# Kernel optimization log

Hardware: AMD Instinct MI355X
Metric: run time of the kernel (lower is better)

## Reference

```python
import jax, jax.numpy as jnp
import numpy as np

B, L, D = 4, 4096, 1024
H, W = 16, 64          # n_heads, window_size
HD = D // H            # head_dim
EPS = 1e-5


def setup_inputs() -> dict:
    key = jax.random.key(0)
    ks = jax.random.split(key, 3)
    s = 1.0 / np.sqrt(D)
    x = jax.random.normal(ks[0], (B, L, D), dtype=jnp.float32)
    Wqkv = (jax.random.normal(ks[1], (3 * D, D), dtype=jnp.float32) * s)
    bqkv = jnp.zeros((3 * D,), dtype=jnp.float32)
    Wproj = (jax.random.normal(ks[2], (D, D), dtype=jnp.float32) * s)
    bproj = jnp.zeros((D,), dtype=jnp.float32)
    gamma = jnp.ones((D,), dtype=jnp.float32)
    beta = jnp.zeros((D,), dtype=jnp.float32)
    return {"x": x, "Wqkv": Wqkv, "bqkv": bqkv, "Wproj": Wproj,
            "bproj": bproj, "gamma": gamma, "beta": beta}


def reference(x, Wqkv, bqkv, Wproj, bproj, gamma, beta):
    scale = HD ** -0.5
    nw = L // W  # L is a multiple of W, so pad_len == 0 (same math as padded path)
    # QKV projection -> [3, B, H, L, HD]
    qkv = (x @ Wqkv.T + bqkv).reshape(B, L, 3, H, HD).transpose(2, 0, 3, 1, 4)
    q, k, v = qkv[0], qkv[1], qkv[2]
    # split into non-overlapping windows: [B, H, nw, W, HD]
    q = q.reshape(B, H, nw, W, HD)
    k = k.reshape(B, H, nw, W, HD)
    v = v.reshape(B, H, nw, W, HD)
    attn = jax.nn.softmax(jnp.einsum('bhnqd,bhnkd->bhnqk', q, k) * scale, axis=-1)
    out = jnp.einsum('bhnqk,bhnkd->bhnqd', attn, v)  # dropout is identity in eval
    out = out.reshape(B, H, L, HD).transpose(0, 2, 1, 3).reshape(B, L, D)
    out = out @ Wproj.T + bproj
    y = out + x
    mean = jnp.mean(y, axis=-1, keepdims=True)
    var = jnp.mean((y - mean) ** 2, axis=-1, keepdims=True)
    return (y - mean) * jax.lax.rsqrt(var + EPS) * gamma + beta
```

## Files before the change

kernel.cpp:

```cpp
#include <hip/hip_runtime.h>
#include <stdint.h>


typedef __attribute__((ext_vector_type(8))) short short8;
typedef __attribute__((ext_vector_type(4))) float float4v;
typedef unsigned short us;

#define GAS const __attribute__((address_space(1))) void
#define LAS __attribute__((address_space(3))) void

__device__ __forceinline__ float bf2f(us u) {
  return __uint_as_float(((unsigned int)u) << 16);
}
__device__ __forceinline__ us f2bf(float f) {
  unsigned int u = __float_as_uint(f);
  unsigned int r = u + 0x7FFFu + ((u >> 16) & 1u);
  return (us)(r >> 16);
}
__device__ __forceinline__ int4 stage8(const float* p) {
  float4 a = *(const float4*)p;
  float4 b = *(const float4*)(p + 4);
  int4 r;
  us* u = (us*)&r;
  u[0] = f2bf(a.x); u[1] = f2bf(a.y); u[2] = f2bf(a.z); u[3] = f2bf(a.w);
  u[4] = f2bf(b.x); u[5] = f2bf(b.y); u[6] = f2bf(b.z); u[7] = f2bf(b.w);
  return r;
}
__device__ __forceinline__ int4 stage8(const us* p) { return *(const int4*)p; }
__device__ __forceinline__ void stc(us* p, float v) { *p = f2bf(v); }
__device__ __forceinline__ void stc(float* p, float v) { *p = v; }

__global__ __launch_bounds__(256) void cast_bf16(const float* __restrict__ src,
                                                 us* __restrict__ dst, int n8) {
  const int i = blockIdx.x * 256 + threadIdx.x;
  if (i < n8) *(int4*)(dst + (size_t)i * 8) = stage8(src + (size_t)i * 8);
}

template <int N, int K, int EPI, int HM, typename CT>
__global__ __launch_bounds__(512, 1) void gemm256(
    const us* __restrict__ A, const us* __restrict__ Bt,
    const float* __restrict__ bias, const float* __restrict__ resid,
    CT* __restrict__ C) {
  __shared__ __align__(16) us As[2][256 * 64];
  __shared__ __align__(16) us Bs[2][256 * 64];
  const int tid = threadIdx.x;
  const int lane = tid & 63;
  const int wave = tid >> 6;
  const int wm = wave >> 2;
  const int wn = wave & 3;
  const int lr = lane & 15, lq = lane >> 4;
  const int m0 = blockIdx.y * 256;
  const int n0 = blockIdx.x * 256;
  const int trow = tid >> 3;
  const int tcol = (((tid & 7) ^ (trow & 7)) * 8);

  constexpr int NT = K / 64;

  float4v acc[8][4];
#pragma unroll
  for (int i = 0; i < 8; i++)
#pragma unroll
    for (int j = 0; j < 4; j++) acc[i][j] = (float4v)0.0f;

#define STAGE256(buf, t)                                                       \
  do {                                                                         \
    const size_t kof = (size_t)(t) * 64;                                       \
    _Pragma("unroll") for (int q = 0; q < 4; q++) {                            \
      const us* ga = A + (size_t)(m0 + q * 64 + trow) * K + kof + tcol;        \
      __builtin_amdgcn_global_load_lds((GAS*)ga,                               \
          (LAS*)&As[buf][(q * 512 + tid) * 8], 16, 0, 0);                      \
    }                                                                          \
    _Pragma("unroll") for (int q = 0; q < 4; q++) {                            \
      const us* gb = Bt + (size_t)(n0 + q * 64 + trow) * K + kof + tcol;       \
      __builtin_amdgcn_global_load_lds((GAS*)gb,                               \
          (LAS*)&Bs[buf][(q * 512 + tid) * 8], 16, 0, 0);                      \
    }                                                                          \
  } while (0)

  STAGE256(0, 0);

  for (int t = 0; t < NT; t++) {
    const int cur = t & 1;
    __builtin_amdgcn_s_barrier();
    if (t + 1 < NT) {
      STAGE256(cur ^ 1, t + 1);
      asm volatile("s_waitcnt vmcnt(8)" ::: "memory");
    } else {
      asm volatile("s_waitcnt vmcnt(0)" ::: "memory");
    }
    __builtin_amdgcn_s_barrier();

    const us* Ab = As[cur];
    const us* Bb = Bs[cur];
#pragma unroll
    for (int kk8 = 0; kk8 < 2; kk8++) {
      short8 bf8[4];
#pragma unroll
      for (int nt = 0; nt < 4; nt++) {
        const int row = wn * 64 + nt * 16 + lr;
        bf8[nt] = *(const short8*)&Bb[row * 64 + (((kk8 * 4 + lq) ^ (lr & 7)) * 8)];
      }
#pragma unroll
      for (int mh = 0; mh < 2; mh++) {
        short8 af[4];
#pragma unroll
        for (int mt = 0; mt < 4; mt++) {
          const int row = wm * 128 + mh * 64 + mt * 16 + lr;
          af[mt] = *(const short8*)&Ab[row * 64 + (((kk8 * 4 + lq) ^ (lr & 7)) * 8)];
        }
        __builtin_amdgcn_s_setprio(1);
#pragma unroll
        for (int mt = 0; mt < 4; mt++)
#pragma unroll
          for (int nt = 0; nt < 4; nt++)
            acc[mh * 4 + mt][nt] = __builtin_amdgcn_mfma_f32_16x16x32_bf16(
                af[mt], bf8[nt], acc[mh * 4 + mt][nt], 0, 0, 0);
        __builtin_amdgcn_s_setprio(0);
      }
    }
  }
#undef STAGE256

  float bb[4];
#pragma unroll
  for (int nt = 0; nt < 4; nt++) bb[nt] = bias[n0 + wn * 64 + nt * 16 + lr];
#pragma unroll
  for (int mh = 0; mh < 2; mh++)
#pragma unroll
    for (int mt = 0; mt < 4; mt++) {
      const int rbase = m0 + wm * 128 + mh * 64 + mt * 16 + lq * 4;
#pragma unroll
      for (int nt = 0; nt < 4; nt++) {
        const int col = n0 + wn * 64 + nt * 16 + lr;
#pragma unroll
        for (int r = 0; r < 4; r++) {
          float v = acc[mh * 4 + mt][nt][r] + bb[nt];
          const int row = rbase + r;
          size_t idx;
          if (HM) {
            const int mat = col >> 10, hh = (col >> 6) & 15, d = col & 63;
            idx = (size_t)mat * (16384u * 1024u) +
                  (size_t)((row >> 12) * 16 + hh) * (4096u * 64u) +
                  (size_t)(row & 4095) * 64 + d;
          } else {
            idx = (size_t)row * N + col;
          }
          if (EPI) v += resid[idx];
          stc(&C[idx], v);
        }
      }
    }
}

__global__ __launch_bounds__(256) void attn_mfma(
    const us* __restrict__ qkv, us* __restrict__ attn) {
  __shared__ __align__(16) us Vt[64 * 64];
  __shared__ __align__(16) us Pl[4 * 16 * 64];
  const int wid = blockIdx.x;
  const int wi = wid & 63;
  const int h = (wid >> 6) & 15;
  const int b = wid >> 10;
  const int tid = threadIdx.x;
  const int lane = tid & 63;
  const int w = tid >> 6;
  const int lr = lane & 15, lq = lane >> 4;
  const int rowbase = b * 4096 + wi * 64;

  const us* Qb = qkv + (size_t)(b * 16 + h) * (4096u * 64u) + (size_t)wi * 4096;
  const us* Kb = Qb + (size_t)16384 * 1024;
  const us* Vb = Kb + (size_t)16384 * 1024;

  {
    const int r = lane;
    const int cs = w * 16;
    const us* vsrc = Vb + (size_t)r * 64 + cs;
    int4 v0 = *(const int4*)vsrc;
    int4 v1 = *(const int4*)(vsrc + 8);
    const us* vv0 = (const us*)&v0;
    const us* vv1 = (const us*)&v1;
#pragma unroll
    for (int i = 0; i < 8; i++) {
      const int d = cs + i;
      Vt[d * 64 + (((r >> 3) ^ (d & 7)) * 8) + (r & 7)] = vv0[i];
    }
#pragma unroll
    for (int i = 0; i < 8; i++) {
      const int d = cs + 8 + i;
      Vt[d * 64 + (((r >> 3) ^ (d & 7)) * 8) + (r & 7)] = vv1[i];
    }
  }

  short8 aq[2];
  {
    const us* qrow = Qb + (size_t)(w * 16 + lr) * 64 + lq * 8;
    aq[0] = *(const short8*)qrow;
    aq[1] = *(const short8*)(qrow + 32);
  }
  float4v s[4];
#pragma unroll
  for (int nt = 0; nt < 4; nt++) s[nt] = (float4v)0.0f;
#pragma unroll
  for (int kk8 = 0; kk8 < 2; kk8++) {
#pragma unroll
    for (int nt = 0; nt < 4; nt++) {
      const us* krow = Kb + (size_t)(nt * 16 + lr) * 64 + kk8 * 32 + lq * 8;
      short8 bk = *(const short8*)krow;
      s[nt] = __builtin_amdgcn_mfma_f32_16x16x32_bf16(aq[kk8], bk, s[nt], 0, 0, 0);
    }
  }

  float p[4][4];
#pragma unroll
  for (int r = 0; r < 4; r++) {
    float mx = -1e30f;
#pragma unroll
    for (int nt = 0; nt < 4; nt++) {
      s[nt][r] *= 0.125f;
      mx = fmaxf(mx, s[nt][r]);
    }
    mx = fmaxf(mx, __shfl_xor(mx, 1));
    mx = fmaxf(mx, __shfl_xor(mx, 2));
    mx = fmaxf(mx, __shfl_xor(mx, 4));
    mx = fmaxf(mx, __shfl_xor(mx, 8));
    float sum = 0.f;
#pragma unroll
    for (int nt = 0; nt < 4; nt++) {
      p[nt][r] = __expf(s[nt][r] - mx);
      sum += p[nt][r];
    }
    sum += __shfl_xor(sum, 1);
    sum += __shfl_xor(sum, 2);
    sum += __shfl_xor(sum, 4);
    sum += __shfl_xor(sum, 8);
    const float inv = 1.0f / sum;
#pragma unroll
    for (int nt = 0; nt < 4; nt++) p[nt][r] *= inv;
  }

  us* pw = Pl + w * 1024;
#pragma unroll
  for (int nt = 0; nt < 4; nt++) {
    const int c = nt * 16 + lr;
#pragma unroll
    for (int r = 0; r < 4; r++) {
      const int row = lq * 4 + r;
      pw[row * 64 + (((c >> 3) ^ (row & 7)) * 8) + (c & 7)] = f2bf(p[nt][r]);
    }
  }
  __syncthreads();

  float4v o[4];
#pragma unroll
  for (int nt = 0; nt < 4; nt++) o[nt] = (float4v)0.0f;
#pragma unroll
  for (int kk8 = 0; kk8 < 2; kk8++) {
    short8 pa = *(const short8*)&pw[lr * 64 + (((lq + kk8 * 4) ^ (lr & 7)) * 8)];
#pragma unroll
    for (int nt = 0; nt < 4; nt++) {
      const int d = nt * 16 + lr;
      short8 vb = *(const short8*)&Vt[d * 64 + (((lq + kk8 * 4) ^ (d & 7)) * 8)];
      o[nt] = __builtin_amdgcn_mfma_f32_16x16x32_bf16(pa, vb, o[nt], 0, 0, 0);
    }
  }

#pragma unroll
  for (int nt = 0; nt < 4; nt++) {
    const int d = nt * 16 + lr;
#pragma unroll
    for (int r = 0; r < 4; r++) {
      const int tok = rowbase + w * 16 + lq * 4 + r;
      attn[(size_t)tok * 1024 + h * 64 + d] = f2bf(o[nt][r]);
    }
  }
}

template <int N, int K, int EPI, typename AT, typename CT>
__global__ __launch_bounds__(256) void gemm_bt(
    const AT* __restrict__ A, const float* __restrict__ Bt,
    const float* __restrict__ bias, const float* __restrict__ resid,
    CT* __restrict__ C) {
  __shared__ __align__(16) us As[128 * 64];
  __shared__ __align__(16) us Bs[128 * 64];
  const int tid = threadIdx.x;
  const int lane = tid & 63;
  const int wave = tid >> 6;
  const int wm = wave >> 1, wn = wave & 1;
  const int lr = lane & 15, lq = lane >> 4;
  const int m0 = blockIdx.y * 128;
  const int n0 = blockIdx.x * 128;
  const int trow = tid >> 3;
  const int tcol = (tid & 7) * 8;

  float4v acc[4][4];
#pragma unroll
  for (int i = 0; i < 4; i++)
#pragma unroll
    for (int j = 0; j < 4; j++) acc[i][j] = (float4v)0.0f;

  for (int k0 = 0; k0 < K; k0 += 64) {
    int4 av[4], bv[4];
#pragma unroll
    for (int p = 0; p < 4; p++) {
      av[p] = stage8(A + (size_t)(m0 + p * 32 + trow) * K + k0 + tcol);
      bv[p] = stage8(Bt + (size_t)(n0 + p * 32 + trow) * K + k0 + tcol);
    }
#pragma unroll
    for (int p = 0; p < 4; p++) {
      *(int4*)&As[(p * 256 + tid) * 8] = av[p];
      *(int4*)&Bs[(p * 256 + tid) * 8] = bv[p];
    }
    __syncthreads();
#pragma unroll
    for (int kk = 0; kk < 64; kk += 32) {
      short8 af[4], bfv[4];
#pragma unroll
      for (int mt = 0; mt < 4; mt++)
        af[mt] = *(const short8*)&As[(wm * 64 + mt * 16 + lr) * 64 + kk + lq * 8];
#pragma unroll
      for (int nt = 0; nt < 4; nt++)
        bfv[nt] = *(const short8*)&Bs[(wn * 64 + nt * 16 + lr) * 64 + kk + lq * 8];
#pragma unroll
      for (int mt = 0; mt < 4; mt++)
#pragma unroll
        for (int nt = 0; nt < 4; nt++)
          acc[mt][nt] = __builtin_amdgcn_mfma_f32_16x16x32_bf16(
              af[mt], bfv[nt], acc[mt][nt], 0, 0, 0);
    }
    __syncthreads();
  }

  float bb[4];
#pragma unroll
  for (int nt = 0; nt < 4; nt++) bb[nt] = bias[n0 + wn * 64 + nt * 16 + lr];
#pragma unroll
  for (int mt = 0; mt < 4; mt++) {
    const int rbase = m0 + wm * 64 + mt * 16 + lq * 4;
#pragma unroll
    for (int nt = 0; nt < 4; nt++) {
      const int col = n0 + wn * 64 + nt * 16 + lr;
#pragma unroll
      for (int r = 0; r < 4; r++) {
        float v = acc[mt][nt][r] + bb[nt];
        size_t idx = (size_t)(rbase + r) * N + col;
        if (EPI) v += resid[idx];
        stc(&C[idx], v);
      }
    }
  }
}

__global__ __launch_bounds__(256) void attn_win(
    const us* __restrict__ qkv, us* __restrict__ attn) {
  __shared__ float qs[64][65];
  __shared__ float ks[64][65];
  __shared__ float vs[64][65];
  const int wid = blockIdx.x;
  const int wi = wid & 63;
  const int h = (wid >> 6) & 15;
  const int b = wid >> 10;
  const int t = threadIdx.x;
  const int rowbase = b * 4096 + wi * 64;
  {
    const int r = t >> 2;
    const int cs = (t & 3) * 16;
    const us* base = qkv + (size_t)(rowbase + r) * 3072 + h * 64 + cs;
#pragma unroll
    for (int s = 0; s < 3; s++) {
      float* dst = (s == 0) ? &qs[r][cs] : (s == 1) ? &ks[r][cs] : &vs[r][cs];
      const us* src = base + s * 1024;
#pragma unroll
      for (int half = 0; half < 2; half++) {
        int4 dv = *(const int4*)(src + half * 8);
        const us* tp = (const us*)&dv;
#pragma unroll
        for (int i = 0; i < 8; i++) dst[half * 8 + i] = bf2f(tp[i]);
      }
    }
  }
  __syncthreads();
  const int r0 = (t >> 4) * 4;
  const int c0 = (t & 15) * 4;
  float acc[4][4] = {};
#pragma unroll 8
  for (int k = 0; k < 64; k++) {
    float qv[4], kv[4];
#pragma unroll
    for (int i = 0; i < 4; i++) qv[i] = qs[r0 + i][k];
#pragma unroll
    for (int j = 0; j < 4; j++) kv[j] = ks[c0 + j][k];
#pragma unroll
    for (int i = 0; i < 4; i++)
#pragma unroll
      for (int j = 0; j < 4; j++) acc[i][j] += qv[i] * kv[j];
  }
  __syncthreads();
#pragma unroll
  for (int i = 0; i < 4; i++)
#pragma unroll
    for (int j = 0; j < 4; j++) qs[r0 + i][c0 + j] = acc[i][j] * 0.125f;
  __syncthreads();
  {
    const int rr = t >> 2;
    const int cs = (t & 3) * 16;
    float pv[16];
    float m = -1e30f;
#pragma unroll
    for (int i = 0; i < 16; i++) {
      pv[i] = qs[rr][cs + i];
      m = fmaxf(m, pv[i]);
    }
    m = fmaxf(m, __shfl_xor(m, 1));
    m = fmaxf(m, __shfl_xor(m, 2));
    float ssum = 0.f;
#pragma unroll
    for (int i = 0; i < 16; i++) {
      pv[i] = __expf(pv[i] - m);
      ssum += pv[i];
    }
    ssum += __shfl_xor(ssum, 1);
    ssum += __shfl_xor(ssum, 2);
    const float inv = 1.0f / ssum;
#pragma unroll
    for (int i = 0; i < 16; i++) qs[rr][cs + i] = pv[i] * inv;
  }
  __syncthreads();
  float o[4][4] = {};
#pragma unroll 8
  for (int k = 0; k < 64; k++) {
    float pr[4], vv[4];
#pragma unroll
    for (int i = 0; i < 4; i++) pr[i] = qs[r0 + i][k];
#pragma unroll
    for (int j = 0; j < 4; j++) vv[j] = vs[k][c0 + j];
#pragma unroll
    for (int i = 0; i < 4; i++)
#pragma unroll
      for (int j = 0; j < 4; j++) o[i][j] += pr[i] * vv[j];
  }
#pragma unroll
  for (int i = 0; i < 4; i++)
#pragma unroll
    for (int j = 0; j < 4; j++)
      attn[(size_t)(rowbase + r0 + i) * 1024 + h * 64 + c0 + j] = f2bf(o[i][j]);
}

__global__ __launch_bounds__(256) void ln_inplace(
    float* __restrict__ y, const float* __restrict__ gamma,
    const float* __restrict__ beta) {
  const int row = blockIdx.x;
  const int t = threadIdx.x;
  float* yr = y + (size_t)row * 1024;
  float4 v = *(const float4*)(yr + t * 4);
  float s1 = v.x + v.y + v.z + v.w;
  float s2 = v.x * v.x + v.y * v.y + v.z * v.z + v.w * v.w;
#pragma unroll
  for (int off = 32; off > 0; off >>= 1) {
    s1 += __shfl_down(s1, off);
    s2 += __shfl_down(s2, off);
  }
  __shared__ float red[8];
  const int lane = t & 63, wave = t >> 6;
  if (lane == 0) {
    red[wave] = s1;
    red[4 + wave] = s2;
  }
  __syncthreads();
  if (t == 0) {
    red[0] = red[0] + red[1] + red[2] + red[3];
    red[4] = red[4] + red[5] + red[6] + red[7];
  }
  __syncthreads();
  const float mean = red[0] * (1.0f / 1024.0f);
  const float var = red[4] * (1.0f / 1024.0f) - mean * mean;
  const float rstd = rsqrtf(var + 1e-5f);
  float4 g = *(const float4*)(gamma + t * 4);
  float4 bt = *(const float4*)(beta + t * 4);
  float4 o;
  o.x = (v.x - mean) * rstd * g.x + bt.x;
  o.y = (v.y - mean) * rstd * g.y + bt.y;
  o.z = (v.z - mean) * rstd * g.z + bt.z;
  o.w = (v.w - mean) * rstd * g.w + bt.w;
  *(float4*)(yr + t * 4) = o;
}

extern "C" void kernel_launch(void* const* d_in, const int* in_sizes, int n_in,
                              void* d_out, int out_size, void* d_ws,
                              size_t ws_size, hipStream_t stream) {
  const float* x = (const float*)d_in[0];
  const float* Wqkv = (const float*)d_in[1];
  const float* bqkv = (const float*)d_in[2];
  const float* Wproj = (const float*)d_in[3];
  const float* bproj = (const float*)d_in[4];
  const float* gamma = (const float*)d_in[5];
  const float* beta = (const float*)d_in[6];
  float* out = (float*)d_out;

  us* qkv = (us*)d_ws;
  us* attn = qkv + (size_t)16384 * 3072;
  us* xb = attn + (size_t)16384 * 1024;
  us* Wqkvb = xb + (size_t)16384 * 1024;
  us* Wprojb = Wqkvb + (size_t)3072 * 1024;
  const size_t need =
      ((size_t)16384 * 3072 + 3 * (size_t)16384 * 1024 + (size_t)3072 * 1024 +
       (size_t)1024 * 1024) * sizeof(us);

  if (ws_size >= need) {
    cast_bf16<<<(16384 * 1024 / 8 + 255) / 256, 256, 0, stream>>>(x, xb,
                                                                  16384 * 128);
    cast_bf16<<<(3072 * 1024 / 8 + 255) / 256, 256, 0, stream>>>(Wqkv, Wqkvb,
                                                                 3072 * 128);
    cast_bf16<<<(1024 * 1024 / 8 + 255) / 256, 256, 0, stream>>>(Wproj, Wprojb,
                                                                 1024 * 128);
    gemm256<3072, 1024, 0, 1, us><<<dim3(12, 64), 512, 0, stream>>>(
        xb, Wqkvb, bqkv, nullptr, qkv);
    attn_mfma<<<4096, 256, 0, stream>>>(qkv, attn);
    gemm256<1024, 1024, 1, 0, float><<<dim3(4, 64), 512, 0, stream>>>(
        attn, Wprojb, bproj, x, out);
  } else {
    gemm_bt<3072, 1024, 0, float, us><<<dim3(24, 128), 256, 0, stream>>>(
        x, Wqkv, bqkv, nullptr, qkv);
    attn_win<<<4096, 256, 0, stream>>>(qkv, attn);
    gemm_bt<1024, 1024, 1, us, float><<<dim3(8, 128), 256, 0, stream>>>(
        attn, Wproj, bproj, x, out);
  }
  ln_inplace<<<16384, 256, 0, stream>>>(out, gamma, beta);
}
```

Before: 354.5 us.

## Shrink GEMM tiles to 128x128 with grouped block swizzle; batch attention windows per block

Replaces the 256x256x64 tile, 512-thread GEMM with a 128x128x32 tile, 256-thread version that remaps block ids in an interleaved order for better L2 locality. It also drops the launch bound of one block per CU, so more blocks fit on each CU and the grid has many more blocks. The attention kernel now processes four windows per block in a loop instead of one, cutting the launch count by four. The trade-off is less data reuse per tile, more barrier iterations along K, and serialized work inside each attention block.

```diff
diff --git a/kernel.cpp b/kernel.cpp
--- a/kernel.cpp
+++ b/kernel.cpp
@@ -37,54 +37,60 @@
 }
 
 template <int N, int K, int EPI, int HM, typename CT>
-__global__ __launch_bounds__(512, 1) void gemm256(
+__global__ __launch_bounds__(256) void gemm128(
     const us* __restrict__ A, const us* __restrict__ Bt,
     const float* __restrict__ bias, const float* __restrict__ resid,
     CT* __restrict__ C) {
-  __shared__ __align__(16) us As[2][256 * 64];
-  __shared__ __align__(16) us Bs[2][256 * 64];
+  constexpr int NBX = N / 128;
+  constexpr int NBY = 128;
+  constexpr int NWG = NBX * NBY;
+  __shared__ __align__(16) us As[2][128 * 32];
+  __shared__ __align__(16) us Bs[2][128 * 32];
   const int tid = threadIdx.x;
   const int lane = tid & 63;
   const int wave = tid >> 6;
-  const int wm = wave >> 2;
-  const int wn = wave & 3;
+  const int wm = wave >> 1, wn = wave & 1;
   const int lr = lane & 15, lq = lane >> 4;
-  const int m0 = blockIdx.y * 256;
-  const int n0 = blockIdx.x * 256;
-  const int trow = tid >> 3;
-  const int tcol = (((tid & 7) ^ (trow & 7)) * 8);
-
-  constexpr int NT = K / 64;
-
-  float4v acc[8][4];
-#pragma unroll
-  for (int i = 0; i < 8; i++)
+
+  int id = blockIdx.y * NBX + blockIdx.x;
+  id = (id & 7) * (NWG / 8) + (id >> 3);
+  const int m0 = (id / NBX) * 128;
+  const int n0 = (id % NBX) * 128;
+
+  const int srow = tid >> 2;
+  const int scol = (((tid & 3) ^ (srow & 3)) * 8);
+
+  constexpr int NT = K / 32;
+
+  float4v acc[4][4];
+#pragma unroll
+  for (int i = 0; i < 4; i++)
 #pragma unroll
     for (int j = 0; j < 4; j++) acc[i][j] = (float4v)0.0f;
 
-#define STAGE256(buf, t)                                                       \
+#define STG128(buf, t)                                                         \
   do {                                                                         \
-    const size_t kof = (size_t)(t) * 64;                                       \
-    _Pragma("unroll") for (int q = 0; q < 4; q++) {                            \
-      const us* ga = A + (size_t)(m0 + q * 64 + trow) * K + kof + tcol;        \
+    const size_t kof = (size_t)(t) * 32;                                       \
+    _Pragma("unroll") for (int p = 0; p < 2; p++) {                            \
+      const us* ga = A + (size_t)(m0 + p * 64 + srow) * K + kof + scol;        \
       __builtin_amdgcn_global_load_lds((GAS*)ga,                               \
-          (LAS*)&As[buf][(q * 512 + tid) * 8], 16, 0, 0);                      \
+          (LAS*)&As[buf][(p * 256 + tid) * 8], 16, 0, 0);                      \
     }                                                                          \
-    _Pragma("unroll") for (int q = 0; q < 4; q++) {                            \
-      const us* gb = Bt + (size_t)(n0 + q * 64 + trow) * K + kof + tcol;       \
+    _Pragma("unroll") for (int p = 0; p < 2; p++) {                            \
+      const us* gb = Bt + (size_t)(n0 + p * 64 + srow) * K + kof + scol;       \
       __builtin_amdgcn_global_load_lds((GAS*)gb,                               \
-          (LAS*)&Bs[buf][(q * 512 + tid) * 8], 16, 0, 0);                      \
+          (LAS*)&Bs[buf][(p * 256 + tid) * 8], 16, 0, 0);                      \
     }                                                                          \
   } while (0)
 
-  STAGE256(0, 0);
+  STG128(0, 0);
 
   for (int t = 0; t < NT; t++) {
     const int cur = t & 1;
     __builtin_amdgcn_s_barrier();
     if (t + 1 < NT) {
-      STAGE256(cur ^ 1, t + 1);
-      asm volatile("s_waitcnt vmcnt(8)" ::: "memory");
+      STG128(cur ^ 1, t + 1);
+      asm volatile("s_waitcnt vmcnt(4)" ::: "memory");
     } else {
       asm volatile("s_waitcnt vmcnt(0)" ::: "memory");
     }
@@ -92,185 +98,181 @@
 
     const us* Ab = As[cur];
     const us* Bb = Bs[cur];
-#pragma unroll
-    for (int kk8 = 0; kk8 < 2; kk8++) {
-      short8 bf8[4];
-#pragma unroll
-      for (int nt = 0; nt < 4; nt++) {
-        const int row = wn * 64 + nt * 16 + lr;
-        bf8[nt] = *(const short8*)&Bb[row * 64 + (((kk8 * 4 + lq) ^ (lr & 7)) * 8)];
-      }
-#pragma unroll
-      for (int mh = 0; mh < 2; mh++) {
-        short8 af[4];
-#pragma unroll
-        for (int mt = 0; mt < 4; mt++) {
-          const int row = wm * 128 + mh * 64 + mt * 16 + lr;
-          af[mt] = *(const short8*)&Ab[row * 64 + (((kk8 * 4 + lq) ^ (lr & 7)) * 8)];
+    short8 af[4], bf8[4];
+#pragma unroll
+    for (int mt = 0; mt < 4; mt++)
+      af[mt] = *(const short8*)&Ab[(wm * 64 + mt * 16 + lr) * 32 +
+                                   ((lq ^ (lr & 3)) * 8)];
+#pragma unroll
+    for (int nt = 0; nt < 4; nt++)
+      bf8[nt] = *(const short8*)&Bb[(wn * 64 + nt * 16 + lr) * 32 +
+                                    ((lq ^ (lr & 3)) * 8)];
+    __builtin_amdgcn_s_setprio(1);
+#pragma unroll
+    for (int mt = 0; mt < 4; mt++)
+#pragma unroll
+      for (int nt = 0; nt < 4; nt++)
+        acc[mt][nt] = __builtin_amdgcn_mfma_f32_16x16x32_bf16(
+            af[mt], bf8[nt], acc[mt][nt], 0, 0, 0);
+    __builtin_amdgcn_s_setprio(0);
+  }
+#undef STG128
+
+  float bb[4];
+#pragma unroll
+  for (int nt = 0; nt < 4; nt++) bb[nt] = bias[n0 + wn * 64 + nt * 16 + lr];
+#pragma unroll
+  for (int mt = 0; mt < 4; mt++) {
+    const int rbase = m0 + wm * 64 + mt * 16 + lq * 4;
+#pragma unroll
+    for (int nt = 0; nt < 4; nt++) {
+      const int col = n0 + wn * 64 + nt * 16 + lr;
+#pragma unroll
+      for (int r = 0; r < 4; r++) {
+        float v = acc[mt][nt][r] + bb[nt];
+        const int row = rbase + r;
+        size_t idx;
+        if (HM) {
+          const int mat = col >> 10, hh = (col >> 6) & 15, d = col & 63;
+          idx = (size_t)mat * (16384u * 1024u) +
+                (size_t)((row >> 12) * 16 + hh) * (4096u * 64u) +
+                (size_t)(row & 4095) * 64 + d;
+        } else {
+          idx = (size_t)row * N + col;
         }
-        __builtin_amdgcn_s_setprio(1);
-#pragma unroll
-        for (int mt = 0; mt < 4; mt++)
-#pragma unroll
-          for (int nt = 0; nt < 4; nt++)
-            acc[mh * 4 + mt][nt] = __builtin_amdgcn_mfma_f32_16x16x32_bf16(
-                af[mt], bf8[nt], acc[mh * 4 + mt][nt], 0, 0, 0);
-        __builtin_amdgcn_s_setprio(0);
-      }
-    }
-  }
-#undef STAGE256
-
-  float bb[4];
-#pragma unroll
-  for (int nt = 0; nt < 4; nt++) bb[nt] = bias[n0 + wn * 64 + nt * 16 + lr];
-#pragma unroll
-  for (int mh = 0; mh < 2; mh++)
-#pragma unroll
-    for (int mt = 0; mt < 4; mt++) {
-      const int rbase = m0 + wm * 128 + mh * 64 + mt * 16 + lq * 4;
-#pragma unroll
-      for (int nt = 0; nt < 4; nt++) {
-        const int col = n0 + wn * 64 + nt * 16 + lr;
-#pragma unroll
-        for (int r = 0; r < 4; r++) {
-          float v = acc[mh * 4 + mt][nt][r] + bb[nt];
-          const int row = rbase + r;
-          size_t idx;
-          if (HM) {
-            const int mat = col >> 10, hh = (col >> 6) & 15, d = col & 63;
-            idx = (size_t)mat * (16384u * 1024u) +
-                  (size_t)((row >> 12) * 16 + hh) * (4096u * 64u) +
-                  (size_t)(row & 4095) * 64 + d;
-          } else {
-            idx = (size_t)row * N + col;
-          }
-          if (EPI) v += resid[idx];
-          stc(&C[idx], v);
-        }
-      }
-    }
+        if (EPI) v += resid[idx];
+        stc(&C[idx], v);
+      }
+    }
+  }
 }
 
 __global__ __launch_bounds__(256) void attn_mfma(
     const us* __restrict__ qkv, us* __restrict__ attn) {
   __shared__ __align__(16) us Vt[64 * 64];
   __shared__ __align__(16) us Pl[4 * 16 * 64];
-  const int wid = blockIdx.x;
-  const int wi = wid & 63;
-  const int h = (wid >> 6) & 15;
-  const int b = wid >> 10;
+  const int g0 = blockIdx.x * 4;
+  const int h = (g0 >> 6) & 15;
+  const int b = g0 >> 10;
   const int tid = threadIdx.x;
   const int lane = tid & 63;
   const int w = tid >> 6;
   const int lr = lane & 15, lq = lane >> 4;
-  const int rowbase = b * 4096 + wi * 64;
-
-  const us* Qb = qkv + (size_t)(b * 16 + h) * (4096u * 64u) + (size_t)wi * 4096;
-  const us* Kb = Qb + (size_t)16384 * 1024;
-  const us* Vb = Kb + (size_t)16384 * 1024;
-
-  {
-    const int r = lane;
-    const int cs = w * 16;
-    const us* vsrc = Vb + (size_t)r * 64 + cs;
-    int4 v0 = *(const int4*)vsrc;
-    int4 v1 = *(const int4*)(vsrc + 8);
-    const us* vv0 = (const us*)&v0;
-    const us* vv1 = (const us*)&v1;
-#pragma unroll
-    for (int i = 0; i < 8; i++) {
-      const int d = cs + i;
-      Vt[d * 64 + (((r >> 3) ^ (d & 7)) * 8) + (r & 7)] = vv0[i];
-    }
-#pragma unroll
-    for (int i = 0; i < 8; i++) {
-      const int d = cs + 8 + i;
-      Vt[d * 64 + (((r >> 3) ^ (d & 7)) * 8) + (r & 7)] = vv1[i];
-    }
-  }
-
-  short8 aq[2];
-  {
-    const us* qrow = Qb + (size_t)(w * 16 + lr) * 64 + lq * 8;
-    aq[0] = *(const short8*)qrow;
-    aq[1] = *(const short8*)(qrow + 32);
-  }
-  float4v s[4];
-#pragma unroll
-  for (int nt = 0; nt < 4; nt++) s[nt] = (float4v)0.0f;
-#pragma unroll
-  for (int kk8 = 0; kk8 < 2; kk8++) {
+
+  const us* Qh = qkv + (size_t)(b * 16 + h) * (4096u * 64u);
+  const us* Kh = Qh + (size_t)16384 * 1024;
+  const us* Vh = Kh + (size_t)16384 * 1024;
+
+  for (int i = 0; i < 4; i++) {
+    const int wi = (g0 + i) & 63;
+    const int rowbase = b * 4096 + wi * 64;
+    const us* Qb = Qh + (size_t)wi * 4096;
+    const us* Kb = Kh + (size_t)wi * 4096;
+    const us* Vb = Vh + (size_t)wi * 4096;
+
+    {
+      const int r = lane;
+      const int cs = w * 16;
+      const us* vsrc = Vb + (size_t)r * 64 + cs;
+      int4 v0 = *(const int4*)vsrc;
+      int4 v1 = *(const int4*)(vsrc + 8);
+      const us* vv0 = (const us*)&v0;
+      const us* vv1 = (const us*)&v1;
+#pragma unroll
+      for (int k = 0; k < 8; k++) {
+        const int d = cs + k;
+        Vt[d * 64 + (((r >> 3) ^ (d & 7)) * 8) + (r & 7)] = vv0[k];
+      }
+#pragma unroll
+      for (int k = 0; k < 8; k++) {
+        const int d = cs + 8 + k;
+        Vt[d * 64 + (((r >> 3) ^ (d & 7)) * 8) + (r & 7)] = vv1[k];
+      }
+    }
+
+    short8 aq[2];
+    {
+      const us* qrow = Qb + (size_t)(w * 16 + lr) * 64 + lq * 8;
+      aq[0] = *(const short8*)qrow;
+      aq[1] = *(const short8*)(qrow + 32);
+    }
+    float4v s[4];
+#pragma unroll
+    for (int nt = 0; nt < 4; nt++) s[nt] = (float4v)0.0f;
+#pragma unroll
+    for (int kk8 = 0; kk8 < 2; kk8++) {
+#pragma unroll
+      for (int nt = 0; nt < 4; nt++) {
+        const us* krow = Kb + (size_t)(nt * 16 + lr) * 64 + kk8 * 32 + lq * 8;
+        short8 bk = *(const short8*)krow;
+        s[nt] = __builtin_amdgcn_mfma_f32_16x16x32_bf16(aq[kk8], bk, s[nt], 0, 0, 0);
+      }
+    }
+
+    float p[4][4];
+#pragma unroll
+    for (int r = 0; r < 4; r++) {
+      float mx = -1e30f;
+#pragma unroll
+      for (int nt = 0; nt < 4; nt++) {
+        s[nt][r] *= 0.125f;
+        mx = fmaxf(mx, s[nt][r]);
+      }
+      mx = fmaxf(mx, __shfl_xor(mx, 1));
+      mx = fmaxf(mx, __shfl_xor(mx, 2));
+      mx = fmaxf(mx, __shfl_xor(mx, 4));
+      mx = fmaxf(mx, __shfl_xor(mx, 8));
+      float sum = 0.f;
+#pragma unroll
+      for (int nt = 0; nt < 4; nt++) {
+        p[nt][r] = __expf(s[nt][r] - mx);
+        sum += p[nt][r];
+      }
+      sum += __shfl_xor(sum, 1);
+      sum += __shfl_xor(sum, 2);
+      sum += __shfl_xor(sum, 4);
+      sum += __shfl_xor(sum, 8);
+      const float inv = 1.0f / sum;
+#pragma unroll
+      for (int nt = 0; nt < 4; nt++) p[nt][r] *= inv;
+    }
+
+    us* pw = Pl + w * 1024;
 #pragma unroll
     for (int nt = 0; nt < 4; nt++) {
-      const us* krow = Kb + (size_t)(nt * 16 + lr) * 64 + kk8 * 32 + lq * 8;
-      short8 bk = *(const short8*)krow;
-      s[nt] = __builtin_amdgcn_mfma_f32_16x16x32_bf16(aq[kk8], bk, s[nt], 0, 0, 0);
-    }
-  }
-
-  float p[4][4];
-#pragma unroll
-  for (int r = 0; r < 4; r++) {
-    float mx = -1e30f;
-#pragma unroll
-    for (int nt = 0; nt < 4; nt++) {
-      s[nt][r] *= 0.125f;
-      mx = fmaxf(mx, s[nt][r]);
-    }
-    mx = fmaxf(mx, __shfl_xor(mx, 1));
-    mx = fmaxf(mx, __shfl_xor(mx, 2));
-    mx = fmaxf(mx, __shfl_xor(mx, 4));
-    mx = fmaxf(mx, __shfl_xor(mx, 8));
-    float sum = 0.f;
-#pragma unroll
-    for (int nt = 0; nt < 4; nt++) {
-      p[nt][r] = __expf(s[nt][r] - mx);
-      sum += p[nt][r];
-    }
-    sum += __shfl_xor(sum, 1);
-    sum += __shfl_xor(sum, 2);
-    sum += __shfl_xor(sum, 4);
-    sum += __shfl_xor(sum, 8);
-    const float inv = 1.0f / sum;
-#pragma unroll
-    for (int nt = 0; nt < 4; nt++) p[nt][r] *= inv;
-  }
-
-  us* pw = Pl + w * 1024;
-#pragma unroll
-  for (int nt = 0; nt < 4; nt++) {
-    const int c = nt * 16 + lr;
-#pragma unroll
-    for (int r = 0; r < 4; r++) {
-      const int row = lq * 4 + r;
-      pw[row * 64 + (((c >> 3) ^ (row & 7)) * 8) + (c & 7)] = f2bf(p[nt][r]);
-    }
-  }
-  __syncthreads();
-
-  float4v o[4];
-#pragma unroll
-  for (int nt = 0; nt < 4; nt++) o[nt] = (float4v)0.0f;
-#pragma unroll
-  for (int kk8 = 0; kk8 < 2; kk8++) {
-    short8 pa = *(const short8*)&pw[lr * 64 + (((lq + kk8 * 4) ^ (lr & 7)) * 8)];
+      const int c = nt * 16 + lr;
+#pragma unroll
+      for (int r = 0; r < 4; r++) {
+        const int row = lq * 4 + r;
+        pw[row * 64 + (((c >> 3) ^ (row & 7)) * 8) + (c & 7)] = f2bf(p[nt][r]);
+      }
+    }
+    __syncthreads();
+
+    float4v o[4];
+#pragma unroll
+    for (int nt = 0; nt < 4; nt++) o[nt] = (float4v)0.0f;
+#pragma unroll
+    for (int kk8 = 0; kk8 < 2; kk8++) {
+      short8 pa = *(const short8*)&pw[lr * 64 + (((lq + kk8 * 4) ^ (lr & 7)) * 8)];
+#pragma unroll
+      for (int nt = 0; nt < 4; nt++) {
+        const int d = nt * 16 + lr;
+        short8 vb = *(const short8*)&Vt[d * 64 + (((lq + kk8 * 4) ^ (d & 7)) * 8)];
+        o[nt] = __builtin_amdgcn_mfma_f32_16x16x32_bf16(pa, vb, o[nt], 0, 0, 0);
+      }
+    }
+
 #pragma unroll
     for (int nt = 0; nt < 4; nt++) {
       const int d = nt * 16 + lr;
-      short8 vb = *(const short8*)&Vt[d * 64 + (((lq + kk8 * 4) ^ (d & 7)) * 8)];
-      o[nt] = __builtin_amdgcn_mfma_f32_16x16x32_bf16(pa, vb, o[nt], 0, 0, 0);
-    }
-  }
-
-#pragma unroll
-  for (int nt = 0; nt < 4; nt++) {
-    const int d = nt * 16 + lr;
-#pragma unroll
-    for (int r = 0; r < 4; r++) {
-      const int tok = rowbase + w * 16 + lq * 4 + r;
-      attn[(size_t)tok * 1024 + h * 64 + d] = f2bf(o[nt][r]);
-    }
+#pragma unroll
+      for (int r = 0; r < 4; r++) {
+        const int tok = rowbase + w * 16 + lq * 4 + r;
+        attn[(size_t)tok * 1024 + h * 64 + d] = f2bf(o[nt][r]);
+      }
+    }
+    if (i < 3) __syncthreads();
   }
 }
 
@@ -511,10 +513,10 @@
                                                                  3072 * 128);
     cast_bf16<<<(1024 * 1024 / 8 + 255) / 256, 256, 0, stream>>>(Wproj, Wprojb,
                                                                  1024 * 128);
-    gemm256<3072, 1024, 0, 1, us><<<dim3(12, 64), 512, 0, stream>>>(
+    gemm128<3072, 1024, 0, 1, us><<<dim3(24, 128), 256, 0, stream>>>(
         xb, Wqkvb, bqkv, nullptr, qkv);
-    attn_mfma<<<4096, 256, 0, stream>>>(qkv, attn);
-    gemm256<1024, 1024, 1, 0, float><<<dim3(4, 64), 512, 0, stream>>>(
+    attn_mfma<<<1024, 256, 0, stream>>>(qkv, attn);
+    gemm128<1024, 1024, 1, 0, float><<<dim3(8, 128), 256, 0, stream>>>(
         attn, Wprojb, bproj, x, out);
   } else {
     gemm_bt<3072, 1024, 0, float, us><<<dim3(24, 128), 256, 0, stream>>>(
```

After: 426.2 us. +20.2%, slower.
